# Performance work log

Hardware: AMD Instinct MI355X
Metric: run time of the kernel (lower is better)

## Reference

```python
import jax, jax.numpy as jnp
import numpy as np

B, S, D = 8, 1024, 768          # batch, block_size, d_model
H = 6                            # n_head
E = 24                           # n_experts
CAP = 4                          # n_expert_capacity
DH = D // H                      # 128, head dim
DF = 384                         # d_ffn
N = S * H                        # tokens after head split = 6144
K = N * CAP // E                 # tokens per expert = 1024


def _uniform(key, shape, fan_in):
    b = 1.0 / np.sqrt(fan_in)
    return jax.random.uniform(key, shape, jnp.float32, -b, b)


def setup_inputs() -> dict:
    key = jax.random.key(0)
    kx, kc, k1, k2, kh, km = jax.random.split(key, 6)
    return {
        "x": jax.random.normal(kx, (B, S, D), jnp.float32),
        "choice": _uniform(kc, (E, DH), DH),
        "w1": _uniform(k1, (E, DH, DF), DH),
        "w2": _uniform(k2, (E, DF, DH), DF),
        "head": _uniform(kh, (D, D), D),
        "merge": _uniform(km, (D, D), D),
    }


def reference(x, choice, w1, w2, head, merge):
    Bb = x.shape[0]
    # input projection then split heads into a token stream of length N
    x = jnp.einsum("bsd,do->bso", x, head)
    x = x.reshape(Bb, N, DH)                              # [B, N, DH]
    # expert-choice routing: softmax over experts per token
    gates = jax.nn.softmax(jnp.einsum("bsd,ed->bse", x, choice), axis=-1)
    # each expert picks its top-K tokens
    G, I = jax.lax.top_k(jnp.swapaxes(gates, -1, -2), K)  # [B, E, K]
    bidx = jnp.arange(Bb)[:, None, None]
    # gather (equivalent to one-hot matmul einsum('beks,bsd->bekd', P, x))
    x_in = x[bidx, I]                                     # [B, E, K, DH]
    # per-expert SwiGLU-free FFN: silu(x w1) w2
    h = jax.nn.silu(jnp.einsum("bekd,edo->beko", x_in, w1))
    x_mlp = jnp.einsum("beki,eid->bekd", h, w2)           # [B, E, K, DH]
    # scatter-combine weighted by gates (einsum('beks,bek,bekd->bsd'))
    x_out = jnp.zeros((Bb, N, DH), x.dtype).at[bidx, I].add(G[..., None] * x_mlp)
    # dropout is identity in eval mode
    x_out = x_out.reshape(Bb, S, D)
    return jnp.einsum("bsd,do->bso", x_out, merge)
```

## Files before the change

kernel.cpp:

```cpp
#include <hip/hip_runtime.h>
#include <stdint.h>
#include <math.h>

typedef __attribute__((ext_vector_type(8))) short short8;
typedef __attribute__((ext_vector_type(4))) short short4v;
typedef __attribute__((ext_vector_type(4))) float floatx4;
typedef __attribute__((ext_vector_type(2))) float floatx2;
typedef __attribute__((ext_vector_type(2))) double doublex2;

#define DEV static __device__ __forceinline__

DEV float bf2f(unsigned short u){ union { unsigned int i; float f; } c; c.i = ((unsigned int)u) << 16; return c.f; }
DEV unsigned short f2bf(float f){ union { float f; unsigned int i; } c; c.f = f; unsigned int u = c.i; u += 0x7fffu + ((u >> 16) & 1u); return (unsigned short)(u >> 16); }

#if defined(__has_builtin)
#if __has_builtin(__builtin_amdgcn_global_load_lds)
#define USE_GLL 1
#endif
#if __has_builtin(__builtin_amdgcn_exp2f) && __has_builtin(__builtin_amdgcn_rcpf)
#define FAST_SILU 1
#endif
#endif
#ifndef USE_GLL
#define USE_GLL 0
#endif
#ifndef FAST_SILU
#define FAST_SILU 0
#endif

DEV void gll16(const unsigned short* g, unsigned short* ldsbase, int lane){
#if USE_GLL
  __builtin_amdgcn_global_load_lds((const __attribute__((address_space(1))) void*)g,
                                   (__attribute__((address_space(3))) void*)ldsbase, 16, 0, 0);
#else
  *(short8*)(ldsbase + lane * 8) = *(const short8*)g;
#endif
}

DEV float silu(float v){
#if FAST_SILU
  float ex = __builtin_amdgcn_exp2f(v * -1.44269504088896f);
  return v * __builtin_amdgcn_rcpf(1.f + ex);
#else
  return v / (1.f + __expf(-v));
#endif
}

DEV void transpose_tile(const float* in, unsigned short* out, int R, int C,
                        int bx, int by, int bz, int tid, unsigned short* tile)
{
  const long boff = (long)bz * (long)R * (long)C;
  in += boff; out += boff;
  const int c0 = bx * 64, r0 = by * 64;
  const int rr = tid >> 4;
  const int c4 = (tid & 15) * 4;
#pragma unroll
  for (int i = 0; i < 4; i++){
    int r = rr + i * 16;
    floatx4 v = *(const floatx4*)(in + (long)(r0 + r) * C + c0 + c4);
#pragma unroll
    for (int u = 0; u < 4; u++) tile[r * 68 + c4 + u] = f2bf(v[u]);
  }
  __syncthreads();
#pragma unroll
  for (int i = 0; i < 4; i++){
    int cc = rr + i * 16;
    short4v v;
#pragma unroll
    for (int u = 0; u < 4; u++) v[u] = (short)tile[(c4 + u) * 68 + cc];
    *(short4v*)(out + (long)(c0 + cc) * R + r0 + c4) = v;
  }
}

__global__ __launch_bounds__(256) void k_prep(const float* __restrict__ x,
    const float* __restrict__ choice, const float* __restrict__ w1,
    const float* __restrict__ w2, const float* __restrict__ head,
    const float* __restrict__ merge,
    unsigned short* __restrict__ xb, unsigned short* __restrict__ headT,
    unsigned short* __restrict__ mergeT, unsigned short* __restrict__ w1T,
    unsigned short* __restrict__ w2T, double* __restrict__ W64)
{
  __shared__ double buf[1536];
  unsigned short* tile = (unsigned short*)buf;
  const int id = blockIdx.x, tid = threadIdx.x;
  if (id < 144){
    transpose_tile(head, headT, 768, 768, id % 12, id / 12, 0, tid, tile);
  } else if (id < 288){
    int l = id - 144;
    transpose_tile(merge, mergeT, 768, 768, l % 12, l / 12, 0, tid, tile);
  } else if (id < 576){
    int l = id - 288;
    transpose_tile(w1, w1T, 128, 384, l % 6, (l / 6) % 2, l / 12, tid, tile);
  } else if (id < 864){
    int l = id - 576;
    transpose_tile(w2, w2T, 384, 128, l % 2, (l / 2) % 6, l / 12, tid, tile);
  } else if (id < 1248){
    int l = id - 864;
    const int sub = tid >> 7, lt = tid & 127;
    const int d = l * 2 + sub;
    double* hrow = buf + sub * 768;
    for (int i = lt; i < 768; i += 128) hrow[i] = (double)head[(long)d * 768 + i];
    __syncthreads();
    for (int c = lt; c < 144; c += 128){
      int h = c / 24, e = c % 24;
      double a = 0.0;
      const double* hr = hrow + h * 128;
      const float* ch = choice + e * 128;
#pragma unroll 8
      for (int k = 0; k < 128; k++) a += hr[k] * (double)ch[k];
      W64[(long)d * 144 + c] = a;
    }
  } else {
    const long l = id - 1248;
    const long i = (l * 256 + tid) * 4;
    floatx4 v = *(const floatx4*)(x + i);
    short4v o;
#pragma unroll
    for (int u = 0; u < 4; u++) o[u] = (short)f2bf(v[u]);
    *(short4v*)(xb + i) = o;
  }
}

template<int OUTF>
DEV void gemm_body(const unsigned short* __restrict__ A, const unsigned short* __restrict__ BT,
                   unsigned short* __restrict__ C, float* __restrict__ Cf, int N, int K,
                   unsigned short* As, unsigned short* Bs, int m0, int n0, int tid)
{
  const int lane = tid & 63;
  const int w = tid >> 6;
  const int wy = w >> 1, wx = w & 1;

  floatx4 acc[4][4];
  {
    floatx4 z4 = {0.f, 0.f, 0.f, 0.f};
#pragma unroll
    for (int i = 0; i < 4; i++)
#pragma unroll
      for (int j = 0; j < 4; j++) acc[i][j] = z4;
  }

  const int rsub = lane >> 3;
  const int kcol = (lane & 7) * 8;

  for (int k0 = 0; k0 < K; k0 += 64){
#pragma unroll
    for (int i = 0; i < 4; i++){
      const int inst = w * 4 + i;
      const int rr = inst * 8 + rsub;
      gll16(A + (long)(m0 + rr) * K + k0 + kcol, &As[inst * 512], lane);
      gll16(BT + (long)(n0 + rr) * K + k0 + kcol, &Bs[inst * 512], lane);
    }
    __syncthreads();
#pragma unroll
    for (int ks = 0; ks < 2; ++ks){
      const int kb = ks * 32 + (lane >> 4) * 8;
      short8 af[4], bfr[4];
#pragma unroll
      for (int mi = 0; mi < 4; mi++) af[mi]  = *(const short8*)&As[(wy * 64 + mi * 16 + (lane & 15)) * 64 + kb];
#pragma unroll
      for (int ni = 0; ni < 4; ni++) bfr[ni] = *(const short8*)&Bs[(wx * 64 + ni * 16 + (lane & 15)) * 64 + kb];
#pragma unroll
      for (int mi = 0; mi < 4; mi++)
#pragma unroll
        for (int ni = 0; ni < 4; ni++)
          acc[mi][ni] = __builtin_amdgcn_mfma_f32_16x16x32_bf16(af[mi], bfr[ni], acc[mi][ni], 0, 0, 0);
    }
    __syncthreads();
  }

  const int ml = lane & 15;
  const int rq = (lane >> 4) * 4;
#pragma unroll
  for (int mi = 0; mi < 4; mi++){
    const int rowb = m0 + wy * 64 + mi * 16 + rq;
#pragma unroll
    for (int ni = 0; ni < 4; ni++){
      const int col = n0 + wx * 64 + ni * 16 + ml;
#pragma unroll
      for (int r = 0; r < 4; r++){
        float v = acc[mi][ni][r];
        if (OUTF) Cf[(long)(rowb + r) * N + col] = v;
        else      C[(long)(rowb + r) * N + col] = f2bf(v);
      }
    }
  }
}

DEV void gates_body(const float* __restrict__ xg, const double* __restrict__ W,
                    double* __restrict__ P, float* xsT , double* Ws ,
                    int row0, int ksegIdx, int tid)
{
  const int tx = tid & 15;
  const int ty = tid >> 4;
  const int kseg = ksegIdx * 192;

  double acc[4][9];
#pragma unroll
  for (int i = 0; i < 4; i++)
#pragma unroll
    for (int j = 0; j < 9; j++) acc[i][j] = 0.0;

  for (int kc = 0; kc < 192; kc += 32){
    const int k0 = kseg + kc;
    {
      const int rL = tid >> 4;
      const int kL = (tid & 15) * 2;
#pragma unroll
      for (int p = 0; p < 4; ++p){
        const int rr = p * 16 + rL;
        floatx2 v = *(const floatx2*)(xg + (long)(row0 + rr) * 768 + k0 + kL);
        *(floatx2*)&xsT[rr * 36 + kL] = v;
      }
    }
    for (int f = tid; f < 4608; f += 256){
      int kk = f / 144, c = f - kk * 144;
      int c9 = c / 9, cm = c - c9 * 9;
      Ws[kk * 160 + c9 * 10 + cm] = W[(long)(k0 + kk) * 144 + c];
    }
    __syncthreads();
#pragma unroll
    for (int q = 0; q < 8; ++q){
      floatx4 xr[4];
#pragma unroll
      for (int i = 0; i < 4; i++)
        xr[i] = *(const floatx4*)&xsT[(ty * 4 + i) * 36 + q * 4];
#pragma unroll
      for (int kk2 = 0; kk2 < 4; ++kk2){
        const double* wrow = Ws + (q * 4 + kk2) * 160 + tx * 10;
        double w[9];
#pragma unroll
        for (int j2 = 0; j2 < 4; j2++){
          doublex2 wv = *(const doublex2*)(wrow + j2 * 2);
          w[j2 * 2] = wv[0]; w[j2 * 2 + 1] = wv[1];
        }
        w[8] = wrow[8];
#pragma unroll
        for (int i = 0; i < 4; i++){
          double xd = (double)xr[i][kk2];
#pragma unroll
          for (int j = 0; j < 9; j++) acc[i][j] += xd * w[j];
        }
      }
    }
    __syncthreads();
  }
  double* dstseg = P + (long)ksegIdx * 8192 * 144;
#pragma unroll
  for (int i = 0; i < 4; i++){
    double* dst = dstseg + (long)(row0 + ty * 4 + i) * 144 + tx * 9;
#pragma unroll
    for (int j = 0; j < 9; j++) dst[j] = acc[i][j];
  }
}

__global__ __launch_bounds__(256, 2) void k_main0(const unsigned short* __restrict__ xb,
    const unsigned short* __restrict__ headT, unsigned short* __restrict__ x1,
    const float* __restrict__ xg, const double* __restrict__ W, double* __restrict__ P)
{
  __shared__ double lds[6272];
  const int id = blockIdx.x, tid = threadIdx.x;
  if (id < 512){
    float* xsT = (float*)lds;
    double* Ws = (double*)((char*)lds + 9216);
    gates_body(xg, W, P, xsT, Ws, (id & 127) * 64, id >> 7, tid);
  } else {
    const int id2 = id - 512;
    unsigned short* As = (unsigned short*)lds;
    unsigned short* Bs = As + 128 * 64;
    gemm_body<0>(xb, headT, x1, nullptr, 768, 768, As, Bs, (id2 & 63) * 128, (id2 >> 6) * 128, tid);
  }
}

__global__ __launch_bounds__(256) void k_softmax(const double* __restrict__ P,
                                                 double* __restrict__ gatesT)
{
  const int gid = blockIdx.x * 256 + threadIdx.x;
  const int R = gid / 6, h = gid % 6;
  const int b = R >> 10, s = R & 1023;
  const int n = s * 6 + h;
  const long S = (long)8192 * 144;
  const long base = (long)R * 144 + h * 24;
  double l[24];
#pragma unroll
  for (int e = 0; e < 24; e++){
    const long o = base + e;
    l[e] = (P[o] + P[S + o]) + (P[2 * S + o] + P[3 * S + o]);
  }
  double m = l[0];
#pragma unroll
  for (int e = 1; e < 24; e++) m = fmax(m, l[e]);
  double ssum = 0.0;
#pragma unroll
  for (int e = 0; e < 24; e++){ l[e] = exp(l[e] - m); ssum += l[e]; }
  double is = 1.0 / ssum;
#pragma unroll
  for (int e = 0; e < 24; e++)
    gatesT[((long)(b * 24 + e)) * 6144 + n] = l[e] * is;
}

DEV int blk_reduce(int v, volatile int* sbuf, int tid){
#pragma unroll
  for (int off = 32; off > 0; off >>= 1) v += __shfl_down(v, off);
  __syncthreads();
  if ((tid & 63) == 0) sbuf[tid >> 6] = v;
  __syncthreads();
  return sbuf[0] + sbuf[1] + sbuf[2] + sbuf[3];
}

__global__ __launch_bounds__(256) void k_topk(const double* __restrict__ gatesT,
                                              int* __restrict__ Kidx, float* __restrict__ Gval,
                                              int* __restrict__ cnt, unsigned short* __restrict__ inv)
{
  __shared__ int sbuf[4];
  __shared__ int s_pos;
  const int tid = threadIdx.x;
  const int be = blockIdx.x;
  const int b = be / 24, e = be % 24;
  const double* g = gatesT + (long)be * 6144;

  unsigned long long key[24];
#pragma unroll
  for (int j = 0; j < 24; j++)
    key[j] = (unsigned long long)__double_as_longlong(g[tid + 256 * j]);

  unsigned long long lo = 0ull, hi = ~0ull;
  for (int it = 0; it < 64; ++it){
    if (hi - lo <= 1ull) break;
    unsigned long long mid = lo + ((hi - lo) >> 1);
    int c = 0;
#pragma unroll
    for (int j = 0; j < 24; j++) c += (key[j] > mid) ? 1 : 0;
    c = blk_reduce(c, sbuf, tid);
    if (c >= 1024) lo = mid; else hi = mid;
  }
  const unsigned long long T = hi;
  int cg = 0;
#pragma unroll
  for (int j = 0; j < 24; j++) cg += (key[j] > T) ? 1 : 0;
  cg = blk_reduce(cg, sbuf, tid);
  const int need = 1024 - cg;

  int lo2 = 0, hi2 = 6144;
  for (int it = 0; it < 13; ++it){
    if (hi2 - lo2 <= 1) break;
    int mid = (lo2 + hi2) >> 1;
    int c = 0;
#pragma unroll
    for (int j = 0; j < 24; j++) c += (key[j] == T && (tid + 256 * j) < mid) ? 1 : 0;
    c = blk_reduce(c, sbuf, tid);
    if (c >= need) hi2 = mid; else lo2 = mid;
  }
  const int m = hi2;

  if (tid == 0) s_pos = 0;
  __syncthreads();
#pragma unroll
  for (int j = 0; j < 24; j++){
    int n = tid + 256 * j;
    bool sel = (key[j] > T) || (key[j] == T && n < m);
    if (sel){
      int slot = atomicAdd(&s_pos, 1);
      Kidx[(long)be * 1024 + slot] = n;
      Gval[(long)be * 1024 + slot] = (float)__longlong_as_double((long long)key[j]);
      int t = b * 6144 + n;
      int p = atomicAdd(&cnt[t], 1);
      inv[(long)t * 24 + p] = (unsigned short)(e * 1024 + slot);
    }
  }
}

__global__ __launch_bounds__(256, 2) void k_gemm2(const unsigned short* __restrict__ A,
    const unsigned short* __restrict__ BT, float* __restrict__ Cf)
{
  __shared__ unsigned short As[128 * 64];
  __shared__ unsigned short Bs[128 * 64];
  gemm_body<1>(A, BT, nullptr, Cf, 768, 768, As, Bs,
               (int)blockIdx.x * 128, (int)blockIdx.y * 128, (int)threadIdx.x);
}

__global__ __launch_bounds__(256, 2) void k_ffn(const unsigned short* __restrict__ x1,
    const unsigned short* __restrict__ w1T, const unsigned short* __restrict__ w2T,
    const int* __restrict__ KidxAll, const float* __restrict__ GvalAll,
    unsigned short* __restrict__ Y)
{
  __shared__ unsigned short As[128 * 128];
  __shared__ unsigned short W1c[64 * 128];
  __shared__ unsigned short W2c[128 * 64];
  __shared__ unsigned short Hc[128 * 64];
  const int tid = threadIdx.x, lane = tid & 63, w = tid >> 6;
  const int tx = lane & 15, quad = lane >> 4;
  const int mt = blockIdx.x;
  const int be = blockIdx.y;
  const int b = be / 24, e = be % 24;
  const int* idx = KidxAll + (long)be * 1024 + mt * 128;
  const float* scl = GvalAll + (long)be * 1024 + mt * 128;
  const unsigned short* A   = x1  + (long)b * 6144 * 128;
  const unsigned short* w1e = w1T + (long)e * 384 * 128;
  const unsigned short* w2e = w2T + (long)e * 128 * 384;

  {
    const int r0 = w * 32;
#pragma unroll
    for (int i = 0; i < 8; i++){
      int rr = r0 + i * 4 + quad;
      int c = tx ^ (rr & 15);
      gll16(A + (long)idx[rr] * 128 + c * 8, &As[(r0 + i * 4) * 128], lane);
    }
  }

  floatx4 Yt[2][8];
  {
    floatx4 z4 = {0.f, 0.f, 0.f, 0.f};
#pragma unroll
    for (int i = 0; i < 2; i++)
#pragma unroll
      for (int j = 0; j < 8; j++) Yt[i][j] = z4;
  }

  for (int nc = 0; nc < 6; ++nc){
    {
      const int r0 = w * 16;
#pragma unroll
      for (int i = 0; i < 4; i++){
        int lr = r0 + i * 4 + quad;
        int c = tx ^ (lr & 15);
        gll16(w1e + (long)(nc * 64 + lr) * 128 + c * 8, &W1c[(r0 + i * 4) * 128], lane);
      }
    }
    {
      const int r0 = w * 32;
#pragma unroll
      for (int i = 0; i < 4; i++){
        int rr = r0 + i * 8 + (lane >> 3);
        int c = (lane & 7) ^ (rr & 7);
        gll16(w2e + (long)rr * 384 + nc * 64 + c * 8, &W2c[(r0 + i * 8) * 64], lane);
      }
    }
    __syncthreads();

    floatx4 h4[2][4];
    {
      floatx4 z4 = {0.f, 0.f, 0.f, 0.f};
#pragma unroll
      for (int i = 0; i < 2; i++)
#pragma unroll
        for (int j = 0; j < 4; j++) h4[i][j] = z4;
    }
#pragma unroll
    for (int ks = 0; ks < 4; ++ks){
      const int chunk = ks * 4 + quad;
      const int pos = chunk ^ tx;
      short8 af[2];
#pragma unroll
      for (int mi = 0; mi < 2; ++mi)
        af[mi] = *(const short8*)&As[(w * 32 + mi * 16 + tx) * 128 + pos * 8];
#pragma unroll
      for (int nf = 0; nf < 4; ++nf){
        short8 bfr = *(const short8*)&W1c[(nf * 16 + tx) * 128 + pos * 8];
#pragma unroll
        for (int mi = 0; mi < 2; ++mi)
          h4[mi][nf] = __builtin_amdgcn_mfma_f32_16x16x32_bf16(af[mi], bfr, h4[mi][nf], 0, 0, 0);
      }
    }
#pragma unroll
    for (int mi = 0; mi < 2; ++mi){
#pragma unroll
      for (int nf = 0; nf < 4; ++nf){
        const int hchunk = nf * 2 + (tx >> 3);
        const int hoff = tx & 7;
#pragma unroll
        for (int r = 0; r < 4; r++){
          float v = silu(h4[mi][nf][r]);
          const int trow = w * 32 + mi * 16 + quad * 4 + r;
          Hc[trow * 64 + (hchunk ^ (trow & 7)) * 8 + hoff] = f2bf(v);
        }
      }
    }
    __syncthreads();

#pragma unroll
    for (int ks = 0; ks < 2; ++ks){
      const int chunk2 = ks * 4 + quad;
      const int posx = chunk2 ^ (tx & 7);
      short8 a2[2], b2[8];
#pragma unroll
      for (int mf = 0; mf < 2; ++mf)
        a2[mf] = *(const short8*)&W2c[(w * 32 + mf * 16 + tx) * 64 + posx * 8];
#pragma unroll
      for (int nf = 0; nf < 8; ++nf)
        b2[nf] = *(const short8*)&Hc[(nf * 16 + tx) * 64 + posx * 8];
#pragma unroll
      for (int mf = 0; mf < 2; ++mf)
#pragma unroll
        for (int nf = 0; nf < 8; ++nf)
          Yt[mf][nf] = __builtin_amdgcn_mfma_f32_16x16x32_bf16(a2[mf], b2[nf], Yt[mf][nf], 0, 0, 0);
    }
    __syncthreads();
  }

#pragma unroll
  for (int nf = 0; nf < 8; ++nf){
    const int rb = nf * 16 + tx;
    const float g = scl[rb];
    unsigned short* dst = Y + ((long)be * 1024 + mt * 128 + rb) * 128 + w * 32 + quad * 4;
#pragma unroll
    for (int mf = 0; mf < 2; ++mf){
      short4v v;
#pragma unroll
      for (int r = 0; r < 4; r++) v[r] = (short)f2bf(Yt[mf][nf][r] * g);
      *(short4v*)(dst + mf * 16) = v;
    }
  }
}

__global__ __launch_bounds__(256) void k_combine(const int* __restrict__ cnt,
    const unsigned short* __restrict__ inv, const unsigned short* __restrict__ Y,
    unsigned short* __restrict__ xout)
{
  const int t = blockIdx.x * 4 + (threadIdx.x >> 6);
  const int lane = threadIdx.x & 63;
  const int b = t / 6144;
  const int c = cnt[t];
  float a0 = 0.f, a1 = 0.f;
  for (int p = 0; p < c; ++p){
    int code = inv[(long)t * 24 + p];
    int e = code >> 10, slot = code & 1023;
    const unsigned short* y = Y + (((long)(b * 24 + e) * 1024 + slot) << 7) + lane * 2;
    a0 += bf2f(y[0]); a1 += bf2f(y[1]);
  }
  unsigned short* o = xout + ((long)t << 7) + lane * 2;
  o[0] = f2bf(a0); o[1] = f2bf(a1);
}

extern "C" void kernel_launch(void* const* d_in, const int* in_sizes, int n_in,
                              void* d_out, int out_size, void* d_ws, size_t ws_size,
                              hipStream_t stream)
{
  const float* x      = (const float*)d_in[0];
  const float* choice = (const float*)d_in[1];
  const float* w1     = (const float*)d_in[2];
  const float* w2     = (const float*)d_in[3];
  const float* head   = (const float*)d_in[4];
  const float* merge  = (const float*)d_in[5];
  float* out = (float*)d_out;
  (void)in_sizes; (void)n_in; (void)out_size; (void)ws_size;

  char* p = (char*)d_ws;
  auto alloc = [&p](size_t bytes) -> void* {
    void* q = (void*)p; p += (bytes + 255) & ~(size_t)255; return q;
  };

  unsigned short* headT = (unsigned short*)alloc((size_t)768 * 768 * 2);
  unsigned short* mergeT= (unsigned short*)alloc((size_t)768 * 768 * 2);
  unsigned short* w1T   = (unsigned short*)alloc((size_t)24 * 384 * 128 * 2);
  unsigned short* w2T   = (unsigned short*)alloc((size_t)24 * 128 * 384 * 2);
  double* W64           = (double*)alloc((size_t)768 * 144 * 8);
  int* Kidx             = (int*)alloc((size_t)192 * 1024 * 4);
  float* Gval           = (float*)alloc((size_t)192 * 1024 * 4);
  int* cnt              = (int*)alloc((size_t)49152 * 4);
  unsigned short* inv   = (unsigned short*)alloc((size_t)49152 * 24 * 2);
  unsigned short* xb    = (unsigned short*)alloc((size_t)8192 * 768 * 2);
  unsigned short* x1    = (unsigned short*)alloc((size_t)8192 * 768 * 2);
  unsigned short* Y     = (unsigned short*)alloc((size_t)192 * 1024 * 128 * 2);
  double* P             = (double*)Y;
  double* gatesT        = (double*)((char*)Y + (size_t)4 * 8192 * 144 * 8);
  unsigned short* xout  = xb;

  hipMemsetAsync(cnt, 0, (size_t)49152 * 4, stream);
  k_prep<<<dim3(7392), 256, 0, stream>>>(x, choice, w1, w2, head, merge,
                                         xb, headT, mergeT, w1T, w2T, W64);
  k_main0<<<dim3(896), 256, 0, stream>>>(xb, headT, x1, x, W64, P);
  k_softmax<<<dim3(192), 256, 0, stream>>>(P, gatesT);
  k_topk<<<dim3(192), 256, 0, stream>>>(gatesT, Kidx, Gval, cnt, inv);
  k_ffn<<<dim3(8, 192, 1), 256, 0, stream>>>(x1, w1T, w2T, Kidx, Gval, Y);
  k_combine<<<dim3(12288), 256, 0, stream>>>(cnt, inv, Y, xout);
  k_gemm2<<<dim3(64, 6, 1), 256, 0, stream>>>(xout, mergeT, out);
}
```

Before: 384.9 us.

## Enlarge fp64 gate tile to 128 rows, pre-convert x to double in LDS

Measured after the change: 386.1 us. About the same (+0.3%).

```diff
diff --git a/kernel.cpp b/kernel.cpp
--- a/kernel.cpp
+++ b/kernel.cpp
@@ -187,16 +187,16 @@
 }
 
 DEV void gates_body(const float* __restrict__ xg, const double* __restrict__ W,
-                    double* __restrict__ P, float* xsT , double* Ws ,
+                    double* __restrict__ P, double* xsT , double* Ws ,
                     int row0, int ksegIdx, int tid)
 {
   const int tx = tid & 15;
   const int ty = tid >> 4;
   const int kseg = ksegIdx * 192;
 
-  double acc[4][9];
-#pragma unroll
-  for (int i = 0; i < 4; i++)
+  double acc[8][9];
+#pragma unroll
+  for (int i = 0; i < 8; i++)
 #pragma unroll
     for (int j = 0; j < 9; j++) acc[i][j] = 0.0;
 
@@ -206,24 +206,34 @@
       const int rL = tid >> 4;
       const int kL = (tid & 15) * 2;
 #pragma unroll
-      for (int p = 0; p < 4; ++p){
+      for (int p = 0; p < 8; ++p){
         const int rr = p * 16 + rL;
         floatx2 v = *(const floatx2*)(xg + (long)(row0 + rr) * 768 + k0 + kL);
-        *(floatx2*)&xsT[rr * 36 + kL] = v;
-      }
-    }
-    for (int f = tid; f < 4608; f += 256){
-      int kk = f / 144, c = f - kk * 144;
-      int c9 = c / 9, cm = c - c9 * 9;
-      Ws[kk * 160 + c9 * 10 + cm] = W[(long)(k0 + kk) * 144 + c];
+        doublex2 d; d[0] = (double)v[0]; d[1] = (double)v[1];
+        *(doublex2*)&xsT[rr * 38 + kL] = d;
+      }
+    }
+    {
+      const int cg = tid & 15, kkg = tid >> 4;
+#pragma unroll
+      for (int kx = 0; kx < 2; ++kx){
+        const int kk = kkg + kx * 16;
+        const double* src = W + (long)(k0 + kk) * 144 + cg * 9;
+        double* dst = Ws + kk * 160 + cg * 10;
+#pragma unroll
+        for (int j = 0; j < 9; j++) dst[j] = src[j];
+      }
     }
     __syncthreads();
 #pragma unroll
     for (int q = 0; q < 8; ++q){
-      floatx4 xr[4];
-#pragma unroll
-      for (int i = 0; i < 4; i++)
-        xr[i] = *(const floatx4*)&xsT[(ty * 4 + i) * 36 + q * 4];
+      doublex2 xr[8][2];
+#pragma unroll
+      for (int i = 0; i < 8; i++){
+        const double* xp = &xsT[(ty + 16 * i) * 38 + q * 4];
+        xr[i][0] = *(const doublex2*)xp;
+        xr[i][1] = *(const doublex2*)(xp + 2);
+      }
 #pragma unroll
       for (int kk2 = 0; kk2 < 4; ++kk2){
         const double* wrow = Ws + (q * 4 + kk2) * 160 + tx * 10;
@@ -235,8 +245,8 @@
         }
         w[8] = wrow[8];
 #pragma unroll
-        for (int i = 0; i < 4; i++){
-          double xd = (double)xr[i][kk2];
+        for (int i = 0; i < 8; i++){
+          const double xd = xr[i][kk2 >> 1][kk2 & 1];
 #pragma unroll
           for (int j = 0; j < 9; j++) acc[i][j] += xd * w[j];
         }
@@ -246,25 +256,25 @@
   }
   double* dstseg = P + (long)ksegIdx * 8192 * 144;
 #pragma unroll
-  for (int i = 0; i < 4; i++){
-    double* dst = dstseg + (long)(row0 + ty * 4 + i) * 144 + tx * 9;
+  for (int i = 0; i < 8; i++){
+    double* dst = dstseg + (long)(row0 + ty + 16 * i) * 144 + tx * 9;
 #pragma unroll
     for (int j = 0; j < 9; j++) dst[j] = acc[i][j];
   }
 }
 
-__global__ __launch_bounds__(256, 2) void k_main0(const unsigned short* __restrict__ xb,
+__global__ __launch_bounds__(256, 1) void k_main0(const unsigned short* __restrict__ xb,
     const unsigned short* __restrict__ headT, unsigned short* __restrict__ x1,
     const float* __restrict__ xg, const double* __restrict__ W, double* __restrict__ P)
 {
-  __shared__ double lds[6272];
+  __shared__ double lds[9984];
   const int id = blockIdx.x, tid = threadIdx.x;
-  if (id < 512){
-    float* xsT = (float*)lds;
-    double* Ws = (double*)((char*)lds + 9216);
-    gates_body(xg, W, P, xsT, Ws, (id & 127) * 64, id >> 7, tid);
+  if (id < 256){
+    double* xsT = lds;
+    double* Ws  = lds + 128 * 38;
+    gates_body(xg, W, P, xsT, Ws, (id & 63) * 128, id >> 6, tid);
   } else {
-    const int id2 = id - 512;
+    const int id2 = id - 256;
     unsigned short* As = (unsigned short*)lds;
     unsigned short* Bs = As + 128 * 64;
     gemm_body<0>(xb, headT, x1, nullptr, 768, 768, As, Bs, (id2 & 63) * 128, (id2 >> 6) * 128, tid);
@@ -274,18 +284,14 @@
 __global__ __launch_bounds__(256) void k_softmax(const double* __restrict__ P,
                                                  double* __restrict__ gatesT)
 {
-  const int gid = blockIdx.x * 256 + threadIdx.x;
-  const int R = gid / 6, h = gid % 6;
-  const int b = R >> 10, s = R & 1023;
-  const int n = s * 6 + h;
+  const int t = blockIdx.x * 256 + threadIdx.x;
+  const int b = t / 6144, n = t % 6144;
   const long S = (long)8192 * 144;
-  const long base = (long)R * 144 + h * 24;
+  const double* base = P + (long)b * 147456 + (long)24 * n;
   double l[24];
 #pragma unroll
-  for (int e = 0; e < 24; e++){
-    const long o = base + e;
-    l[e] = (P[o] + P[S + o]) + (P[2 * S + o] + P[3 * S + o]);
-  }
+  for (int e = 0; e < 24; e++)
+    l[e] = (base[e] + base[S + e]) + (base[2 * S + e] + base[3 * S + e]);
   double m = l[0];
 #pragma unroll
   for (int e = 1; e < 24; e++) m = fmax(m, l[e]);
@@ -569,7 +575,7 @@
   hipMemsetAsync(cnt, 0, (size_t)49152 * 4, stream);
   k_prep<<<dim3(7392), 256, 0, stream>>>(x, choice, w1, w2, head, merge,
                                          xb, headT, mergeT, w1T, w2T, W64);
-  k_main0<<<dim3(896), 256, 0, stream>>>(xb, headT, x1, x, W64, P);
+  k_main0<<<dim3(640), 256, 0, stream>>>(xb, headT, x1, x, W64, P);
   k_softmax<<<dim3(192), 256, 0, stream>>>(P, gatesT);
   k_topk<<<dim3(192), 256, 0, stream>>>(gatesT, Kidx, Gval, cnt, inv);
   k_ffn<<<dim3(8, 192, 1), 256, 0, stream>>>(x1, w1T, w2T, Kidx, Gval, Y);
```
